# Kernel tuning notes

Hardware: AMD Instinct MI355X
Metric: run time of the kernel (lower is better)

## Reference

```python
import jax, jax.numpy as jnp
import numpy as np

STALK_DIM = 16
N_NODES = 50000
N_EDGES = 400000
HIDDEN = 64


def setup_inputs() -> dict:
    key = jax.random.key(0)
    k1, k2, k3, k4 = jax.random.split(key, 4)
    d = STALK_DIM
    x = jax.random.normal(k1, (N_NODES, d), dtype=jnp.float32)
    edge_index = jax.random.randint(k2, (2, N_EDGES), 0, N_NODES, dtype=jnp.int64)
    W1 = jax.random.normal(k3, (HIDDEN, 2 * d), dtype=jnp.float32) * (1.0 / np.sqrt(2 * d))
    b1 = jnp.zeros((HIDDEN,), dtype=jnp.float32)
    W2 = jax.random.normal(k4, (d, HIDDEN), dtype=jnp.float32) * (1.0 / np.sqrt(HIDDEN))
    b2 = jnp.zeros((d,), dtype=jnp.float32)
    return {"x": x, "edge_index": edge_index, "W1": W1, "b1": b1, "W2": W2, "b2": b2}


def reference(x, edge_index, W1, b1, W2, b2):
    d = x.shape[1]
    n = x.shape[0]
    src, dst = edge_index[0], edge_index[1]
    xs, xd = x[src], x[dst]  # [E, d]

    def reflection(a, b):
        h = jax.nn.relu(jnp.concatenate([a, b], axis=1) @ W1.T + b1)
        return h @ W2.T + b2  # [E, d]

    def householder(v):
        # F.normalize(v, dim=1): v / max(||v||, 1e-12)
        vn = v / jnp.maximum(jnp.linalg.norm(v, axis=1, keepdims=True), 1e-12)
        return jnp.eye(d, dtype=v.dtype)[None] - 2.0 * vn[:, :, None] * vn[:, None, :]

    F_s = householder(reflection(xs, xd))  # [E, d, d]
    F_d = householder(reflection(xd, xs))  # [E, d, d]
    L_sd = -jnp.einsum('eki,ekj->eij', F_s, F_d)  # -F_s^T @ F_d, [E, d, d]

    # degrees: both endpoints of every edge contribute 1
    ones_e = jnp.ones(src.shape[0], dtype=x.dtype)
    deg = jnp.zeros(n, dtype=x.dtype).at[src].add(ones_e).at[dst].add(ones_e)
    deg_inv_sqrt = 1.0 / jnp.sqrt(jnp.maximum(deg, 1e-5))
    # D_inv_sqrt is scalar*I per node, so normalization is a scalar coefficient per edge
    coef = deg_inv_sqrt[src] * deg_inv_sqrt[dst]  # [E]

    # out[s] -= D^-1/2_s L D^-1/2_d x[d] ; out[d] -= D^-1/2_d L^T D^-1/2_s x[s]
    msg_s = coef[:, None] * jnp.einsum('eij,ej->ei', L_sd, xd)  # goes to src
    msg_d = coef[:, None] * jnp.einsum('eji,ej->ei', L_sd, xs)  # goes to dst

    out = x - jnp.zeros_like(x).at[src].add(msg_s) - jnp.zeros_like(x).at[dst].add(msg_d)
    return jax.nn.relu(out)
```

## Files before the change

kernel.cpp:

```cpp
#include <hip/hip_runtime.h>
#include <hip/hip_bf16.h>

#define N_NODES 50000
#define N_EDGES 400000
#define D 16
#define HID 64

#define SCAN_B 256
#define SCAN_G ((N_NODES + SCAN_B - 1) / SCAN_B)

#define CNT_OFF   0
#define OFF_OFF   (N_NODES)
#define CUR_OFF   (2 * N_NODES + 1)
#define BS_OFF    (3 * N_NODES + 1)
#define BS2_OFF   (BS_OFF + SCAN_B)
#define FLAGS_I   (BS2_OFF + SCAN_B)
#define MSG_OFF   ((FLAGS_I + 2 + 3) & ~3)
#define CSR_NEEDED_BYTES ((size_t)(MSG_OFF + 2 * N_EDGES * D) * 4 + 64)

#define FB_NDEG   (N_NODES)
#define FB_NACC   (N_NODES * D)
#define FB_FLAGS  (FB_NDEG + FB_NACC)

__device__ __forceinline__ float bf_bits(unsigned short us) {
    return __uint_as_float(((unsigned)us) << 16);
}

__device__ __forceinline__ float ld_f(const void* p, int idx, int f32) {
    return f32 ? ((const float*)p)[idx]
               : bf_bits(((const unsigned short*)p)[idx]);
}

__device__ __forceinline__ void load16(const void* __restrict__ p, long long base,
                                       int f32, float* o) {
    if (f32) {
        const float4* q = (const float4*)((const float*)p + base);
        float4 a = q[0], b = q[1], c = q[2], d = q[3];
        o[0]=a.x; o[1]=a.y; o[2]=a.z; o[3]=a.w;
        o[4]=b.x; o[5]=b.y; o[6]=b.z; o[7]=b.w;
        o[8]=c.x; o[9]=c.y; o[10]=c.z; o[11]=c.w;
        o[12]=d.x; o[13]=d.y; o[14]=d.z; o[15]=d.w;
    } else {
        const uint4* q = (const uint4*)((const unsigned short*)p + base);
        uint4 a = q[0], b = q[1];
        unsigned u[8] = {a.x, a.y, a.z, a.w, b.x, b.y, b.z, b.w};
#pragma unroll
        for (int k = 0; k < 8; k++) {
            o[2 * k]     = __uint_as_float(u[k] << 16);
            o[2 * k + 1] = __uint_as_float(u[k] & 0xffff0000u);
        }
    }
}

__device__ __forceinline__ void load_edge(const void* __restrict__ ei, int e, int is64,
                                          int& s, int& d) {
    if (is64) {
        const long long* p = (const long long*)ei;
        s = (int)p[e];
        d = (int)p[N_EDGES + e];
    } else {
        const int* p = (const int*)ei;
        s = p[e];
        d = p[N_EDGES + e];
    }
}

__device__ __forceinline__ void detect_flags(const void* x, const void* ei, int* flags) {
    const unsigned short* h = (const unsigned short*)x;
    int f32 = 0;
    for (int k = 0; k < 256; k++) {
        float v = bf_bits(h[k]);
        if (!(v == v) || fabsf(v) > 1.0e6f) { f32 = 1; break; }
    }
    const long long* p = (const long long*)ei;
    int i64 = 1;
    for (int k = 0; k < 16; k++) {
        long long v = p[k];
        if (v < 0 || v >= N_NODES) { i64 = 0; break; }
    }
    flags[0] = f32;
    flags[1] = i64;
}

__device__ __forceinline__ void edge_math(
    const float* __restrict__ sW1, const float* __restrict__ sW2t,
    const float* __restrict__ sb1, const float* __restrict__ sb2,
    const float* xs, const float* xd, float coef,
    float* ms, float* md)
{
    float vs[D], vd[D];
#pragma unroll
    for (int i = 0; i < D; i++) { vs[i] = sb2[i]; vd[i] = sb2[i]; }

#pragma unroll 4
    for (int j = 0; j < HID; j++) {
        float hs = sb1[j], hd = sb1[j];
        const float* w = &sW1[j * 2 * D];
#pragma unroll
        for (int k = 0; k < D; k++) {
            float w0 = w[k];
            float w1 = w[D + k];
            hs = fmaf(w0, xs[k], hs);
            hs = fmaf(w1, xd[k], hs);
            hd = fmaf(w0, xd[k], hd);
            hd = fmaf(w1, xs[k], hd);
        }
        hs = fmaxf(hs, 0.0f);
        hd = fmaxf(hd, 0.0f);
        const float* w2 = &sW2t[j * D];
#pragma unroll
        for (int i = 0; i < D; i++) {
            vs[i] = fmaf(w2[i], hs, vs[i]);
            vd[i] = fmaf(w2[i], hd, vd[i]);
        }
    }

    float ns = 0.0f, nd = 0.0f;
#pragma unroll
    for (int i = 0; i < D; i++) { ns = fmaf(vs[i], vs[i], ns); nd = fmaf(vd[i], vd[i], nd); }
    float is_ = 1.0f / fmaxf(sqrtf(ns), 1e-12f);
    float id_ = 1.0f / fmaxf(sqrtf(nd), 1e-12f);
#pragma unroll
    for (int i = 0; i < D; i++) { vs[i] *= is_; vd[i] *= id_; }

    float dot1 = 0.0f;
#pragma unroll
    for (int i = 0; i < D; i++) dot1 = fmaf(vd[i], xd[i], dot1);
#pragma unroll
    for (int i = 0; i < D; i++) ms[i] = fmaf(-2.0f * dot1, vd[i], xd[i]);
    float dot2 = 0.0f;
#pragma unroll
    for (int i = 0; i < D; i++) dot2 = fmaf(vs[i], ms[i], dot2);
#pragma unroll
    for (int i = 0; i < D; i++) ms[i] = coef * fmaf(-2.0f * dot2, vs[i], ms[i]);

    float dot3 = 0.0f;
#pragma unroll
    for (int i = 0; i < D; i++) dot3 = fmaf(vs[i], xs[i], dot3);
#pragma unroll
    for (int i = 0; i < D; i++) md[i] = fmaf(-2.0f * dot3, vs[i], xs[i]);
    float dot4 = 0.0f;
#pragma unroll
    for (int i = 0; i < D; i++) dot4 = fmaf(vd[i], md[i], dot4);
#pragma unroll
    for (int i = 0; i < D; i++) md[i] = coef * fmaf(-2.0f * dot4, vd[i], md[i]);
}

__device__ __forceinline__ void stage_weights(
    const void* W1, const void* b1, const void* W2, const void* b2, int f32,
    float* sW1, float* sW2t, float* sb1, float* sb2)
{
    int t = threadIdx.x;
    for (int idx = t; idx < HID * 2 * D; idx += blockDim.x)
        sW1[idx] = ld_f(W1, idx, f32);
    for (int idx = t; idx < HID * D; idx += blockDim.x) {
        int j = idx / D, i = idx % D;
        sW2t[idx] = ld_f(W2, i * HID + j, f32);
    }
    if (t < HID) sb1[t] = ld_f(b1, t, f32);
    if (t < D)  sb2[t] = ld_f(b2, t, f32);
}

__global__ void csr_init_kernel(int* __restrict__ wsI,
                                const void* __restrict__ x,
                                const void* __restrict__ ei) {
    int i = blockIdx.x * blockDim.x + threadIdx.x;
    if (i < N_NODES) wsI[CNT_OFF + i] = 0;
    if (blockIdx.x == 0 && threadIdx.x == 0)
        detect_flags(x, ei, wsI + FLAGS_I);
}

__global__ void csr_count_kernel(const void* __restrict__ ei, int* __restrict__ wsI) {
    int i64 = wsI[FLAGS_I + 1];
    int e = blockIdx.x * blockDim.x + threadIdx.x;
    if (e >= N_EDGES) return;
    int s, d;
    load_edge(ei, e, i64, s, d);
    atomicAdd(&wsI[CNT_OFF + s], 1);
    atomicAdd(&wsI[CNT_OFF + d], 1);
}

__global__ __launch_bounds__(SCAN_B) void csr_scan1_kernel(int* __restrict__ wsI) {
    __shared__ int sm[SCAN_B];
    int t = threadIdx.x;
    int g = blockIdx.x * SCAN_B + t;
    int c = (g < N_NODES) ? wsI[CNT_OFF + g] : 0;
    sm[t] = c;
    __syncthreads();
    for (int st = SCAN_B / 2; st > 0; st >>= 1) {
        if (t < st) sm[t] += sm[t + st];
        __syncthreads();
    }
    if (t == 0) wsI[BS_OFF + blockIdx.x] = sm[0];
}

__global__ __launch_bounds__(SCAN_B) void csr_scan2_kernel(int* __restrict__ wsI) {
    __shared__ int sm[SCAN_B];
    int t = threadIdx.x;
    int v = (t < SCAN_G) ? wsI[BS_OFF + t] : 0;
    sm[t] = v;
    __syncthreads();
    for (int st = 1; st < SCAN_B; st <<= 1) {
        int u = (t >= st) ? sm[t - st] : 0;
        __syncthreads();
        sm[t] += u;
        __syncthreads();
    }
    if (t < SCAN_G) wsI[BS2_OFF + t] = sm[t] - v;
}

__global__ __launch_bounds__(SCAN_B) void csr_scan3_kernel(int* __restrict__ wsI) {
    __shared__ int sm[SCAN_B];
    int t = threadIdx.x;
    int g = blockIdx.x * SCAN_B + t;
    int c = (g < N_NODES) ? wsI[CNT_OFF + g] : 0;
    sm[t] = c;
    __syncthreads();
    for (int st = 1; st < SCAN_B; st <<= 1) {
        int u = (t >= st) ? sm[t - st] : 0;
        __syncthreads();
        sm[t] += u;
        __syncthreads();
    }
    int excl = sm[t] - c + wsI[BS2_OFF + blockIdx.x];
    if (g < N_NODES) {
        wsI[OFF_OFF + g] = excl;
        wsI[CUR_OFF + g] = excl;
        if (g == N_NODES - 1) wsI[OFF_OFF + N_NODES] = excl + c;
    }
}

__global__ __launch_bounds__(256) void csr_edge_kernel(
    const void* __restrict__ x,
    const void* __restrict__ ei,
    const void* __restrict__ W1,
    const void* __restrict__ b1,
    const void* __restrict__ W2,
    const void* __restrict__ b2,
    int* __restrict__ wsI)
{
    __shared__ __align__(16) float sW1[HID * 2 * D];
    __shared__ __align__(16) float sW2t[HID * D];
    __shared__ float sb1[HID];
    __shared__ float sb2[D];

    int f32 = wsI[FLAGS_I];
    int i64 = wsI[FLAGS_I + 1];
    stage_weights(W1, b1, W2, b2, f32, sW1, sW2t, sb1, sb2);
    __syncthreads();

    int e = blockIdx.x * blockDim.x + threadIdx.x;
    if (e >= N_EDGES) return;

    int s, d;
    load_edge(ei, e, i64, s, d);

    float xs[D], xd[D];
    load16(x, (long long)s * D, f32, xs);
    load16(x, (long long)d * D, f32, xd);

    float degs = (float)wsI[CNT_OFF + s];
    float degd = (float)wsI[CNT_OFF + d];
    float coef = (1.0f / sqrtf(fmaxf(degs, 1e-5f))) * (1.0f / sqrtf(fmaxf(degd, 1e-5f)));

    float ms[D], md[D];
    edge_math(sW1, sW2t, sb1, sb2, xs, xd, coef, ms, md);

    float* msg = (float*)(wsI + MSG_OFF);
    int slot_s = atomicAdd(&wsI[CUR_OFF + s], 1);
    float4* m0 = (float4*)(msg + (long long)slot_s * D);
    m0[0] = make_float4(ms[0], ms[1], ms[2], ms[3]);
    m0[1] = make_float4(ms[4], ms[5], ms[6], ms[7]);
    m0[2] = make_float4(ms[8], ms[9], ms[10], ms[11]);
    m0[3] = make_float4(ms[12], ms[13], ms[14], ms[15]);
    int slot_d = atomicAdd(&wsI[CUR_OFF + d], 1);
    float4* m1 = (float4*)(msg + (long long)slot_d * D);
    m1[0] = make_float4(md[0], md[1], md[2], md[3]);
    m1[1] = make_float4(md[4], md[5], md[6], md[7]);
    m1[2] = make_float4(md[8], md[9], md[10], md[11]);
    m1[3] = make_float4(md[12], md[13], md[14], md[15]);
}

__global__ __launch_bounds__(256) void csr_gather_kernel(
    const void* __restrict__ x,
    const int* __restrict__ wsI,
    void* __restrict__ out)
{
    int f32 = wsI[FLAGS_I];
    int n = blockIdx.x * 16 + (threadIdx.x >> 4);
    int i = threadIdx.x & 15;
    if (n >= N_NODES) return;

    const int* off = wsI + OFF_OFF;
    const float* msg = (const float*)(wsI + MSG_OFF);

    int beg = off[n], end = off[n + 1];
    float a = 0.0f;
    for (int it = beg; it < end; it++)
        a += msg[(long long)it * D + i];
    float v = ld_f(x, n * D + i, f32) + a;
    v = fmaxf(v, 0.0f);
    if (f32) ((float*)out)[n * D + i] = v;
    else     ((__hip_bfloat16*)out)[n * D + i] = __float2bfloat16(v);
}

__global__ void fb_init_kernel(float* __restrict__ ws,
                               const void* __restrict__ x,
                               const void* __restrict__ ei) {
    int i = blockIdx.x * blockDim.x + threadIdx.x;
    if (i < FB_FLAGS) ws[i] = 0.0f;
    if (blockIdx.x == 0 && threadIdx.x == 0)
        detect_flags(x, ei, (int*)(ws + FB_FLAGS));
}

__global__ void fb_deg_kernel(const void* __restrict__ ei, float* __restrict__ ws) {
    int i64 = ((const int*)(ws + FB_FLAGS))[1];
    int e = blockIdx.x * blockDim.x + threadIdx.x;
    if (e >= N_EDGES) return;
    int s, d;
    load_edge(ei, e, i64, s, d);
    atomicAdd(&ws[s], 1.0f);
    atomicAdd(&ws[d], 1.0f);
}

__global__ __launch_bounds__(256) void fb_edge_kernel(
    const void* __restrict__ x,
    const void* __restrict__ ei,
    const void* __restrict__ W1,
    const void* __restrict__ b1,
    const void* __restrict__ W2,
    const void* __restrict__ b2,
    float* __restrict__ ws)
{
    __shared__ __align__(16) float sW1[HID * 2 * D];
    __shared__ __align__(16) float sW2t[HID * D];
    __shared__ float sb1[HID];
    __shared__ float sb2[D];

    const int* flags = (const int*)(ws + FB_FLAGS);
    int f32 = flags[0];
    int i64 = flags[1];
    stage_weights(W1, b1, W2, b2, f32, sW1, sW2t, sb1, sb2);
    __syncthreads();

    int e = blockIdx.x * blockDim.x + threadIdx.x;
    if (e >= N_EDGES) return;

    int s, d;
    load_edge(ei, e, i64, s, d);

    float xs[D], xd[D];
    load16(x, (long long)s * D, f32, xs);
    load16(x, (long long)d * D, f32, xd);

    float coef = (1.0f / sqrtf(fmaxf(ws[s], 1e-5f))) * (1.0f / sqrtf(fmaxf(ws[d], 1e-5f)));

    float ms[D], md[D];
    edge_math(sW1, sW2t, sb1, sb2, xs, xd, coef, ms, md);

    float* acc = ws + FB_NDEG;
#pragma unroll
    for (int i = 0; i < D; i++) atomicAdd(&acc[(long long)s * D + i], ms[i]);
#pragma unroll
    for (int i = 0; i < D; i++) atomicAdd(&acc[(long long)d * D + i], md[i]);
}

__global__ void fb_finalize_kernel(const void* __restrict__ x,
                                   const float* __restrict__ ws,
                                   void* __restrict__ out)
{
    int f32 = ((const int*)(ws + FB_FLAGS))[0];
    const float* acc = ws + FB_NDEG;
    int i = blockIdx.x * blockDim.x + threadIdx.x;
    if (i >= FB_NACC) return;
    float v = ld_f(x, i, f32) + acc[i];
    v = fmaxf(v, 0.0f);
    if (f32) ((float*)out)[i] = v;
    else     ((__hip_bfloat16*)out)[i] = __float2bfloat16(v);
}

extern "C" void kernel_launch(void* const* d_in, const int* in_sizes, int n_in,
                              void* d_out, int out_size, void* d_ws, size_t ws_size,
                              hipStream_t stream)
{
    const void* x  = d_in[0];
    const void* ei = d_in[1];
    const void* W1 = d_in[2];
    const void* b1 = d_in[3];
    const void* W2 = d_in[4];
    const void* b2 = d_in[5];

    int blk = 256;
    if (ws_size >= CSR_NEEDED_BYTES) {
        int* wsI = (int*)d_ws;
        csr_init_kernel<<<(N_NODES + blk - 1) / blk, blk, 0, stream>>>(wsI, x, ei);
        csr_count_kernel<<<(N_EDGES + blk - 1) / blk, blk, 0, stream>>>(ei, wsI);
        csr_scan1_kernel<<<SCAN_G, SCAN_B, 0, stream>>>(wsI);
        csr_scan2_kernel<<<1, SCAN_B, 0, stream>>>(wsI);
        csr_scan3_kernel<<<SCAN_G, SCAN_B, 0, stream>>>(wsI);
        csr_edge_kernel<<<(N_EDGES + blk - 1) / blk, blk, 0, stream>>>(x, ei, W1, b1, W2, b2, wsI);
        csr_gather_kernel<<<(N_NODES + 15) / 16, blk, 0, stream>>>(x, wsI, d_out);
    } else {
        float* ws = (float*)d_ws;
        fb_init_kernel<<<(FB_FLAGS + blk - 1) / blk, blk, 0, stream>>>(ws, x, ei);
        fb_deg_kernel<<<(N_EDGES + blk - 1) / blk, blk, 0, stream>>>(ei, ws);
        fb_edge_kernel<<<(N_EDGES + blk - 1) / blk, blk, 0, stream>>>(x, ei, W1, b1, W2, b2, ws);
        fb_finalize_kernel<<<(FB_NACC + blk - 1) / blk, blk, 0, stream>>>(x, ws, d_out);
    }
}
```

Before: 209.7 us.

## Replicate degree counters, fuse scan passes, vectorize weight loads and gather

```diff
diff --git a/kernel.cpp b/kernel.cpp
--- a/kernel.cpp
+++ b/kernel.cpp
@@ -9,26 +9,32 @@
 #define SCAN_B 256
 #define SCAN_G ((N_NODES + SCAN_B - 1) / SCAN_B)
 
-#define CNT_OFF   0
-#define OFF_OFF   (N_NODES)
-#define CUR_OFF   (2 * N_NODES + 1)
-#define BS_OFF    (3 * N_NODES + 1)
-#define BS2_OFF   (BS_OFF + SCAN_B)
-#define FLAGS_I   (BS2_OFF + SCAN_B)
-#define MSG_OFF   ((FLAGS_I + 2 + 3) & ~3)
-#define CSR_NEEDED_BYTES ((size_t)(MSG_OFF + 2 * N_EDGES * D) * 4 + 64)
+typedef unsigned short ushort_t;
+
+#define CNT4_OFF  0
+#define DEG_OFF   (4 * N_NODES)
+#define OFF_OFF   (5 * N_NODES)
+#define CUR_OFF   (6 * N_NODES + 1)
+#define BS_OFF    (7 * N_NODES + 1)
+#define FLAGS_I   (BS_OFF + SCAN_G)
+#define MSG_OFF_I (((FLAGS_I + 2) + 3) & ~3)
+#define CSR_NEEDED_BYTES ((size_t)(MSG_OFF_I + 2 * N_EDGES * D) * 4 + 64)
 
 #define FB_NDEG   (N_NODES)
 #define FB_NACC   (N_NODES * D)
 #define FB_FLAGS  (FB_NDEG + FB_NACC)
 
-__device__ __forceinline__ float bf_bits(unsigned short us) {
+__device__ __forceinline__ float bf_bits(ushort_t us) {
     return __uint_as_float(((unsigned)us) << 16);
 }
-
+__device__ __forceinline__ ushort_t f2bf(float v) {
+    unsigned u = __float_as_uint(v);
+    unsigned r = (u + 0x7fffu + ((u >> 16) & 1u)) >> 16;
+    return (ushort_t)r;
+}
 __device__ __forceinline__ float ld_f(const void* p, int idx, int f32) {
     return f32 ? ((const float*)p)[idx]
-               : bf_bits(((const unsigned short*)p)[idx]);
+               : bf_bits(((const ushort_t*)p)[idx]);
 }
 
 __device__ __forceinline__ void load16(const void* __restrict__ p, long long base,
@@ -41,7 +47,7 @@
         o[8]=c.x; o[9]=c.y; o[10]=c.z; o[11]=c.w;
         o[12]=d.x; o[13]=d.y; o[14]=d.z; o[15]=d.w;
     } else {
-        const uint4* q = (const uint4*)((const unsigned short*)p + base);
+        const uint4* q = (const uint4*)((const ushort_t*)p + base);
         uint4 a = q[0], b = q[1];
         unsigned u[8] = {a.x, a.y, a.z, a.w, b.x, b.y, b.z, b.w};
 #pragma unroll
@@ -66,7 +72,7 @@
 }
 
 __device__ __forceinline__ void detect_flags(const void* x, const void* ei, int* flags) {
-    const unsigned short* h = (const unsigned short*)x;
+    const ushort_t* h = (const ushort_t*)x;
     int f32 = 0;
     for (int k = 0; k < 256; k++) {
         float v = bf_bits(h[k]);
@@ -80,70 +86,6 @@
     }
     flags[0] = f32;
     flags[1] = i64;
-}
-
-__device__ __forceinline__ void edge_math(
-    const float* __restrict__ sW1, const float* __restrict__ sW2t,
-    const float* __restrict__ sb1, const float* __restrict__ sb2,
-    const float* xs, const float* xd, float coef,
-    float* ms, float* md)
-{
-    float vs[D], vd[D];
-#pragma unroll
-    for (int i = 0; i < D; i++) { vs[i] = sb2[i]; vd[i] = sb2[i]; }
-
-#pragma unroll 4
-    for (int j = 0; j < HID; j++) {
-        float hs = sb1[j], hd = sb1[j];
-        const float* w = &sW1[j * 2 * D];
-#pragma unroll
-        for (int k = 0; k < D; k++) {
-            float w0 = w[k];
-            float w1 = w[D + k];
-            hs = fmaf(w0, xs[k], hs);
-            hs = fmaf(w1, xd[k], hs);
-            hd = fmaf(w0, xd[k], hd);
-            hd = fmaf(w1, xs[k], hd);
-        }
-        hs = fmaxf(hs, 0.0f);
-        hd = fmaxf(hd, 0.0f);
-        const float* w2 = &sW2t[j * D];
-#pragma unroll
-        for (int i = 0; i < D; i++) {
-            vs[i] = fmaf(w2[i], hs, vs[i]);
-            vd[i] = fmaf(w2[i], hd, vd[i]);
-        }
-    }
-
-    float ns = 0.0f, nd = 0.0f;
-#pragma unroll
-    for (int i = 0; i < D; i++) { ns = fmaf(vs[i], vs[i], ns); nd = fmaf(vd[i], vd[i], nd); }
-    float is_ = 1.0f / fmaxf(sqrtf(ns), 1e-12f);
-    float id_ = 1.0f / fmaxf(sqrtf(nd), 1e-12f);
-#pragma unroll
-    for (int i = 0; i < D; i++) { vs[i] *= is_; vd[i] *= id_; }
-
-    float dot1 = 0.0f;
-#pragma unroll
-    for (int i = 0; i < D; i++) dot1 = fmaf(vd[i], xd[i], dot1);
-#pragma unroll
-    for (int i = 0; i < D; i++) ms[i] = fmaf(-2.0f * dot1, vd[i], xd[i]);
-    float dot2 = 0.0f;
-#pragma unroll
-    for (int i = 0; i < D; i++) dot2 = fmaf(vs[i], ms[i], dot2);
-#pragma unroll
-    for (int i = 0; i < D; i++) ms[i] = coef * fmaf(-2.0f * dot2, vs[i], ms[i]);
-
-    float dot3 = 0.0f;
-#pragma unroll
-    for (int i = 0; i < D; i++) dot3 = fmaf(vs[i], xs[i], dot3);
-#pragma unroll
-    for (int i = 0; i < D; i++) md[i] = fmaf(-2.0f * dot3, vs[i], xs[i]);
-    float dot4 = 0.0f;
-#pragma unroll
-    for (int i = 0; i < D; i++) dot4 = fmaf(vd[i], md[i], dot4);
-#pragma unroll
-    for (int i = 0; i < D; i++) md[i] = coef * fmaf(-2.0f * dot4, vd[i], md[i]);
 }
 
 __device__ __forceinline__ void stage_weights(
@@ -161,11 +103,88 @@
     if (t < D)  sb2[t] = ld_f(b2, t, f32);
 }
 
+__device__ __forceinline__ void edge_math_v4(
+    const float* __restrict__ sW1, const float* __restrict__ sW2t,
+    const float* __restrict__ sb1, const float* __restrict__ sb2,
+    const float* xs, const float* xd, float coef,
+    float* ms, float* md)
+{
+    float vs[D], vd[D];
+#pragma unroll
+    for (int i = 0; i < D; i++) { vs[i] = sb2[i]; vd[i] = sb2[i]; }
+
+#pragma unroll 4
+    for (int j = 0; j < HID; j++) {
+        float hs = sb1[j], hd = sb1[j];
+        const float4* w4 = (const float4*)&sW1[j * 2 * D];
+#pragma unroll
+        for (int t = 0; t < 4; t++) {
+            float4 wv = w4[t];
+            int k = 4 * t;
+            hs = fmaf(wv.x, xs[k],     hs); hd = fmaf(wv.x, xd[k],     hd);
+            hs = fmaf(wv.y, xs[k + 1], hs); hd = fmaf(wv.y, xd[k + 1], hd);
+            hs = fmaf(wv.z, xs[k + 2], hs); hd = fmaf(wv.z, xd[k + 2], hd);
+            hs = fmaf(wv.w, xs[k + 3], hs); hd = fmaf(wv.w, xd[k + 3], hd);
+        }
+#pragma unroll
+        for (int t = 0; t < 4; t++) {
+            float4 wv = w4[4 + t];
+            int k = 4 * t;
+            hs = fmaf(wv.x, xd[k],     hs); hd = fmaf(wv.x, xs[k],     hd);
+            hs = fmaf(wv.y, xd[k + 1], hs); hd = fmaf(wv.y, xs[k + 1], hd);
+            hs = fmaf(wv.z, xd[k + 2], hs); hd = fmaf(wv.z, xs[k + 2], hd);
+            hs = fmaf(wv.w, xd[k + 3], hs); hd = fmaf(wv.w, xs[k + 3], hd);
+        }
+        hs = fmaxf(hs, 0.0f);
+        hd = fmaxf(hd, 0.0f);
+        const float4* w24 = (const float4*)&sW2t[j * D];
+#pragma unroll
+        for (int t = 0; t < 4; t++) {
+            float4 u = w24[t];
+            int i = 4 * t;
+            vs[i]     = fmaf(u.x, hs, vs[i]);     vd[i]     = fmaf(u.x, hd, vd[i]);
+            vs[i + 1] = fmaf(u.y, hs, vs[i + 1]); vd[i + 1] = fmaf(u.y, hd, vd[i + 1]);
+            vs[i + 2] = fmaf(u.z, hs, vs[i + 2]); vd[i + 2] = fmaf(u.z, hd, vd[i + 2]);
+            vs[i + 3] = fmaf(u.w, hs, vs[i + 3]); vd[i + 3] = fmaf(u.w, hd, vd[i + 3]);
+        }
+    }
+
+    float ns = 0.0f, nd = 0.0f;
+#pragma unroll
+    for (int i = 0; i < D; i++) { ns = fmaf(vs[i], vs[i], ns); nd = fmaf(vd[i], vd[i], nd); }
+    float is_ = 1.0f / fmaxf(sqrtf(ns), 1e-12f);
+    float id_ = 1.0f / fmaxf(sqrtf(nd), 1e-12f);
+#pragma unroll
+    for (int i = 0; i < D; i++) { vs[i] *= is_; vd[i] *= id_; }
+
+    float dot1 = 0.0f;
+#pragma unroll
+    for (int i = 0; i < D; i++) dot1 = fmaf(vd[i], xd[i], dot1);
+#pragma unroll
+    for (int i = 0; i < D; i++) ms[i] = fmaf(-2.0f * dot1, vd[i], xd[i]);
+    float dot2 = 0.0f;
+#pragma unroll
+    for (int i = 0; i < D; i++) dot2 = fmaf(vs[i], ms[i], dot2);
+#pragma unroll
+    for (int i = 0; i < D; i++) ms[i] = coef * fmaf(-2.0f * dot2, vs[i], ms[i]);
+
+    float dot3 = 0.0f;
+#pragma unroll
+    for (int i = 0; i < D; i++) dot3 = fmaf(vs[i], xs[i], dot3);
+#pragma unroll
+    for (int i = 0; i < D; i++) md[i] = fmaf(-2.0f * dot3, vs[i], xs[i]);
+    float dot4 = 0.0f;
+#pragma unroll
+    for (int i = 0; i < D; i++) dot4 = fmaf(vd[i], md[i], dot4);
+#pragma unroll
+    for (int i = 0; i < D; i++) md[i] = coef * fmaf(-2.0f * dot4, vd[i], md[i]);
+}
+
 __global__ void csr_init_kernel(int* __restrict__ wsI,
                                 const void* __restrict__ x,
                                 const void* __restrict__ ei) {
     int i = blockIdx.x * blockDim.x + threadIdx.x;
-    if (i < N_NODES) wsI[CNT_OFF + i] = 0;
+    if (i < 4 * N_NODES) wsI[CNT4_OFF + i] = 0;
     if (blockIdx.x == 0 && threadIdx.x == 0)
         detect_flags(x, ei, wsI + FLAGS_I);
 }
@@ -176,15 +195,21 @@
     if (e >= N_EDGES) return;
     int s, d;
     load_edge(ei, e, i64, s, d);
-    atomicAdd(&wsI[CNT_OFF + s], 1);
-    atomicAdd(&wsI[CNT_OFF + d], 1);
+    int r = (e & 3) * N_NODES;
+    atomicAdd(&wsI[CNT4_OFF + r + s], 1);
+    atomicAdd(&wsI[CNT4_OFF + r + d], 1);
 }
 
 __global__ __launch_bounds__(SCAN_B) void csr_scan1_kernel(int* __restrict__ wsI) {
     __shared__ int sm[SCAN_B];
     int t = threadIdx.x;
     int g = blockIdx.x * SCAN_B + t;
-    int c = (g < N_NODES) ? wsI[CNT_OFF + g] : 0;
+    int c = 0;
+    if (g < N_NODES) {
+        c = wsI[CNT4_OFF + g] + wsI[CNT4_OFF + N_NODES + g]
+          + wsI[CNT4_OFF + 2 * N_NODES + g] + wsI[CNT4_OFF + 3 * N_NODES + g];
+        wsI[DEG_OFF + g] = c;
+    }
     sm[t] = c;
     __syncthreads();
     for (int st = SCAN_B / 2; st > 0; st >>= 1) {
@@ -194,26 +219,23 @@
     if (t == 0) wsI[BS_OFF + blockIdx.x] = sm[0];
 }
 
-__global__ __launch_bounds__(SCAN_B) void csr_scan2_kernel(int* __restrict__ wsI) {
+__global__ __launch_bounds__(SCAN_B) void csr_scan3_kernel(int* __restrict__ wsI) {
+    __shared__ int sB[SCAN_B];
     __shared__ int sm[SCAN_B];
     int t = threadIdx.x;
-    int v = (t < SCAN_G) ? wsI[BS_OFF + t] : 0;
-    sm[t] = v;
+    int bsv = (t < SCAN_G) ? wsI[BS_OFF + t] : 0;
+    sB[t] = bsv;
     __syncthreads();
     for (int st = 1; st < SCAN_B; st <<= 1) {
-        int u = (t >= st) ? sm[t - st] : 0;
+        int u = (t >= st) ? sB[t - st] : 0;
         __syncthreads();
-        sm[t] += u;
+        sB[t] += u;
         __syncthreads();
     }
-    if (t < SCAN_G) wsI[BS2_OFF + t] = sm[t] - v;
-}
-
-__global__ __launch_bounds__(SCAN_B) void csr_scan3_kernel(int* __restrict__ wsI) {
-    __shared__ int sm[SCAN_B];
-    int t = threadIdx.x;
+    int blockBase = sB[blockIdx.x] - wsI[BS_OFF + blockIdx.x];
+
     int g = blockIdx.x * SCAN_B + t;
-    int c = (g < N_NODES) ? wsI[CNT_OFF + g] : 0;
+    int c = (g < N_NODES) ? wsI[DEG_OFF + g] : 0;
     sm[t] = c;
     __syncthreads();
     for (int st = 1; st < SCAN_B; st <<= 1) {
@@ -222,7 +244,7 @@
         sm[t] += u;
         __syncthreads();
     }
-    int excl = sm[t] - c + wsI[BS2_OFF + blockIdx.x];
+    int excl = sm[t] - c + blockBase;
     if (g < N_NODES) {
         wsI[OFF_OFF + g] = excl;
         wsI[CUR_OFF + g] = excl;
@@ -259,14 +281,14 @@
     load16(x, (long long)s * D, f32, xs);
     load16(x, (long long)d * D, f32, xd);
 
-    float degs = (float)wsI[CNT_OFF + s];
-    float degd = (float)wsI[CNT_OFF + d];
+    float degs = (float)wsI[DEG_OFF + s];
+    float degd = (float)wsI[DEG_OFF + d];
     float coef = (1.0f / sqrtf(fmaxf(degs, 1e-5f))) * (1.0f / sqrtf(fmaxf(degd, 1e-5f)));
 
     float ms[D], md[D];
-    edge_math(sW1, sW2t, sb1, sb2, xs, xd, coef, ms, md);
-
-    float* msg = (float*)(wsI + MSG_OFF);
+    edge_math_v4(sW1, sW2t, sb1, sb2, xs, xd, coef, ms, md);
+
+    float* msg = (float*)(wsI + MSG_OFF_I);
     int slot_s = atomicAdd(&wsI[CUR_OFF + s], 1);
     float4* m0 = (float4*)(msg + (long long)slot_s * D);
     m0[0] = make_float4(ms[0], ms[1], ms[2], ms[3]);
@@ -287,21 +309,50 @@
     void* __restrict__ out)
 {
     int f32 = wsI[FLAGS_I];
-    int n = blockIdx.x * 16 + (threadIdx.x >> 4);
-    int i = threadIdx.x & 15;
+    int n = blockIdx.x * 64 + (threadIdx.x >> 2);
+    int c = threadIdx.x & 3;
     if (n >= N_NODES) return;
 
     const int* off = wsI + OFF_OFF;
-    const float* msg = (const float*)(wsI + MSG_OFF);
+    const float4* msg4 = (const float4*)(wsI + MSG_OFF_I);
 
     int beg = off[n], end = off[n + 1];
-    float a = 0.0f;
-    for (int it = beg; it < end; it++)
-        a += msg[(long long)it * D + i];
-    float v = ld_f(x, n * D + i, f32) + a;
-    v = fmaxf(v, 0.0f);
-    if (f32) ((float*)out)[n * D + i] = v;
-    else     ((__hip_bfloat16*)out)[n * D + i] = __float2bfloat16(v);
+    float4 a = make_float4(0.0f, 0.0f, 0.0f, 0.0f);
+    int it = beg;
+    for (; it + 2 <= end; it += 2) {
+        float4 u = msg4[(long long)it * 4 + c];
+        float4 v = msg4[(long long)(it + 1) * 4 + c];
+        a.x += u.x + v.x; a.y += u.y + v.y; a.z += u.z + v.z; a.w += u.w + v.w;
+    }
+    if (it < end) {
+        float4 u = msg4[(long long)it * 4 + c];
+        a.x += u.x; a.y += u.y; a.z += u.z; a.w += u.w;
+    }
+
+    long long xb = (long long)n * D + 4 * c;
+    float4 xv;
+    if (f32) {
+        xv = *(const float4*)((const float*)x + xb);
+    } else {
+        uint2 u = *(const uint2*)((const ushort_t*)x + xb);
+        xv.x = __uint_as_float(u.x << 16);
+        xv.y = __uint_as_float(u.x & 0xffff0000u);
+        xv.z = __uint_as_float(u.y << 16);
+        xv.w = __uint_as_float(u.y & 0xffff0000u);
+    }
+    float4 r;
+    r.x = fmaxf(xv.x + a.x, 0.0f);
+    r.y = fmaxf(xv.y + a.y, 0.0f);
+    r.z = fmaxf(xv.z + a.z, 0.0f);
+    r.w = fmaxf(xv.w + a.w, 0.0f);
+    if (f32) {
+        *(float4*)((float*)out + xb) = r;
+    } else {
+        uint2 o;
+        o.x = (unsigned)f2bf(r.x) | ((unsigned)f2bf(r.y) << 16);
+        o.y = (unsigned)f2bf(r.z) | ((unsigned)f2bf(r.w) << 16);
+        *(uint2*)((ushort_t*)out + xb) = o;
+    }
 }
 
 __global__ void fb_init_kernel(float* __restrict__ ws,
@@ -324,40 +375,29 @@
 }
 
 __global__ __launch_bounds__(256) void fb_edge_kernel(
-    const void* __restrict__ x,
-    const void* __restrict__ ei,
-    const void* __restrict__ W1,
-    const void* __restrict__ b1,
-    const void* __restrict__ W2,
-    const void* __restrict__ b2,
+    const void* __restrict__ x, const void* __restrict__ ei,
+    const void* __restrict__ W1, const void* __restrict__ b1,
+    const void* __restrict__ W2, const void* __restrict__ b2,
     float* __restrict__ ws)
 {
     __shared__ __align__(16) float sW1[HID * 2 * D];
     __shared__ __align__(16) float sW2t[HID * D];
     __shared__ float sb1[HID];
     __shared__ float sb2[D];
-
     const int* flags = (const int*)(ws + FB_FLAGS);
-    int f32 = flags[0];
-    int i64 = flags[1];
+    int f32 = flags[0], i64 = flags[1];
     stage_weights(W1, b1, W2, b2, f32, sW1, sW2t, sb1, sb2);
     __syncthreads();
-
     int e = blockIdx.x * blockDim.x + threadIdx.x;
     if (e >= N_EDGES) return;
-
     int s, d;
     load_edge(ei, e, i64, s, d);
-
     float xs[D], xd[D];
     load16(x, (long long)s * D, f32, xs);
     load16(x, (long long)d * D, f32, xd);
-
     float coef = (1.0f / sqrtf(fmaxf(ws[s], 1e-5f))) * (1.0f / sqrtf(fmaxf(ws[d], 1e-5f)));
-
     float ms[D], md[D];
-    edge_math(sW1, sW2t, sb1, sb2, xs, xd, coef, ms, md);
-
+    edge_math_v4(sW1, sW2t, sb1, sb2, xs, xd, coef, ms, md);
     float* acc = ws + FB_NDEG;
 #pragma unroll
     for (int i = 0; i < D; i++) atomicAdd(&acc[(long long)s * D + i], ms[i]);
@@ -393,13 +433,12 @@
     int blk = 256;
     if (ws_size >= CSR_NEEDED_BYTES) {
         int* wsI = (int*)d_ws;
-        csr_init_kernel<<<(N_NODES + blk - 1) / blk, blk, 0, stream>>>(wsI, x, ei);
+        csr_init_kernel<<<(4 * N_NODES + blk - 1) / blk, blk, 0, stream>>>(wsI, x, ei);
         csr_count_kernel<<<(N_EDGES + blk - 1) / blk, blk, 0, stream>>>(ei, wsI);
         csr_scan1_kernel<<<SCAN_G, SCAN_B, 0, stream>>>(wsI);
-        csr_scan2_kernel<<<1, SCAN_B, 0, stream>>>(wsI);
         csr_scan3_kernel<<<SCAN_G, SCAN_B, 0, stream>>>(wsI);
         csr_edge_kernel<<<(N_EDGES + blk - 1) / blk, blk, 0, stream>>>(x, ei, W1, b1, W2, b2, wsI);
-        csr_gather_kernel<<<(N_NODES + 15) / 16, blk, 0, stream>>>(x, wsI, d_out);
+        csr_gather_kernel<<<(N_NODES + 63) / 64, blk, 0, stream>>>(x, wsI, d_out);
     } else {
         float* ws = (float*)d_ws;
         fb_init_kernel<<<(FB_FLAGS + blk - 1) / blk, blk, 0, stream>>>(ws, x, ei);
```

Result: faster. 201.4 us (-4.0%).
